# Performance work log

Measured on AMD Instinct MI355X. Metric: run time of the kernel, lower is better.

## Reference

```python
import jax, jax.numpy as jnp
import numpy as np

N, D, H = 1024, 256, 512


def _linear_init(key, fan_in, fan_out):
    kw, kb = jax.random.split(key)
    bound = 1.0 / np.sqrt(fan_in)
    w = jax.random.uniform(kw, (fan_in, fan_out), jnp.float32, -bound, bound)
    b = jax.random.uniform(kb, (fan_out,), jnp.float32, -bound, bound)
    return w, b


def setup_inputs() -> dict:
    key = jax.random.key(0)
    ks = jax.random.split(key, 8)
    domain_a = jax.random.normal(ks[0], (N, D), jnp.float32)
    domain_b = jax.random.normal(ks[1], (N, D), jnp.float32)
    mu_w0, mu_b0 = _linear_init(ks[2], D, H)
    mu_w1, mu_b1 = _linear_init(ks[3], H, H)
    mu_w2, mu_b2 = _linear_init(ks[4], H, D)
    lv_w0, lv_b0 = _linear_init(ks[5], D, H)
    lv_w1, lv_b1 = _linear_init(ks[6], H, H)
    lv_w2, lv_b2 = _linear_init(ks[7], H, D)
    return dict(domain_a=domain_a, domain_b=domain_b,
                mu_w0=mu_w0, mu_b0=mu_b0, mu_w1=mu_w1, mu_b1=mu_b1, mu_w2=mu_w2, mu_b2=mu_b2,
                lv_w0=lv_w0, lv_b0=lv_b0, lv_w1=lv_w1, lv_b1=lv_b1, lv_w2=lv_w2, lv_b2=lv_b2)


def _net(x, ws, bs, final_act):
    h = x
    for i in range(len(ws)):
        h = h @ ws[i] + bs[i]
        if i < len(ws) - 1:
            h = jax.nn.relu(h)
    return final_act(h)


def _l2norm(h):
    # L2NormEncoder == F.normalize(dim=-1), eps clamp like torch
    n = jnp.maximum(jnp.linalg.norm(h, axis=-1, keepdims=True), 1e-12)
    return h / n


def reference(domain_a, domain_b, mu_w0, mu_b0, mu_w1, mu_b1, mu_w2, mu_b2,
              lv_w0, lv_b0, lv_w1, lv_b1, lv_w2, lv_b2):
    mu_ws, mu_bs = [mu_w0, mu_w1, mu_w2], [mu_b0, mu_b1, mu_b2]
    lv_ws, lv_bs = [lv_w0, lv_w1, lv_w2], [lv_b0, lv_b1, lv_b2]

    # ---- embedding-model loss: prob-model params frozen (requires_grad=False) ----
    sg = jax.lax.stop_gradient
    mu = _net(domain_a, [sg(w) for w in mu_ws], [sg(b) for b in mu_bs], _l2norm)
    log_var = _net(domain_a, [sg(w) for w in lv_ws], [sg(b) for b in lv_bs], jnp.tanh)
    inv_var = jnp.exp(-log_var)                                  # [N, D]
    pos_probs = jnp.sum(-(domain_b - mu) ** 2 * inv_var - log_var, axis=-1)  # [N]
    # pairwise: [i, j, d] = b[j, d] - mu[i, d]; mean over j
    diff2_mean = jnp.mean((domain_b[None, :, :] - mu[:, None, :]) ** 2, axis=1)  # [N, D]
    neg_probs = jnp.sum(-diff2_mean * inv_var - log_var, axis=-1)  # [N]
    embed_model_loss = jnp.mean(pos_probs - neg_probs)

    # ---- prob-model loss: embeddings detached, params trainable ----
    a_d, b_d = sg(domain_a), sg(domain_b)
    mu2 = _net(a_d, mu_ws, mu_bs, _l2norm)
    lv2 = _net(a_d, lv_ws, lv_bs, jnp.tanh)
    prob_model_loss = jnp.mean(jnp.sum((b_d - mu2) ** 2 * jnp.exp(-lv2) + lv2, axis=-1))

    emb_coef, prob_coef = 1.0, 1.0
    loss = emb_coef * embed_model_loss + prob_coef * prob_model_loss
    return loss
```

## Files before the change

kernel.cpp:

```cpp
#include <hip/hip_runtime.h>
#include <hip/hip_fp16.h>

#define N_ROWS 1024
#define DIM 256
#define HID 512
#define CTR 16

typedef _Float16 half_t;
typedef __attribute__((ext_vector_type(4))) _Float16 half4v;
typedef __attribute__((ext_vector_type(8))) _Float16 half8v;
typedef __attribute__((ext_vector_type(16))) float f32x16;

struct Params {
    const float* a;
    const float* b;
    const float* w[6];
    const float* bias[6];
    unsigned* c1;
    unsigned* c2;
    unsigned* c3;
    float* acc;
    unsigned* done;
    float* zbase;
    float* part_s;
    float* part_s2;
    unsigned short* g_mu;
    unsigned short* g_lv;
    half_t* g_h1[2];
    half_t* g_h2[2];
    half_t* wt[6];
    float* out;
};

__global__ __launch_bounds__(256) void prep_kernel(Params p) {
    const int y = blockIdx.y, bx = blockIdx.x, tid = threadIdx.x;

    if (y == 6) {
        if (bx < 64) {
            const int d = tid, r0 = bx * 16;
            float s = 0.f, s2 = 0.f;
            #pragma unroll
            for (int r = 0; r < 16; ++r) {
                float v = p.b[(r0 + r) * DIM + d];
                s += v; s2 = fmaf(v, v, s2);
            }
            p.part_s[bx * 256 + d] = s;
            p.part_s2[bx * 256 + d] = s2;
        } else if (bx == 64) {
            #pragma unroll
            for (int k = 0; k < 12; ++k) p.zbase[tid + k * 256] = 0.f;
        }
        return;
    }
    __shared__ float T[32][33];
    const float* src = p.w[y];
    half_t* dst = p.wt[y];
    const int K = (y < 2) ? DIM : HID;
    const int N = (y < 4) ? HID : DIM;
    const int C = K >> 5;
    const int tilesN = N >> 5;
    if (bx >= C * tilesN) return;
    const int tk = bx / tilesN, tn = bx % tilesN;

    {
        const int r = tid >> 3, c4 = (tid & 7) * 4;
        float4 v = *(const float4*)&src[(tk * 32 + r) * N + tn * 32 + c4];
        T[r][c4 + 0] = v.x; T[r][c4 + 1] = v.y; T[r][c4 + 2] = v.z; T[r][c4 + 3] = v.w;
    }
    __syncthreads();
    const int which = tid >> 7;
    const int lane64 = (tid >> 1) & 63;
    const int epart = tid & 1;
    const int hi = lane64 >> 5, lr = lane64 & 31;
    const int rbase = which * 16 + hi * 8 + epart * 4;
    half4v h;
    h[0] = (half_t)T[rbase + 0][lr];
    h[1] = (half_t)T[rbase + 1][lr];
    h[2] = (half_t)T[rbase + 2][lr];
    h[3] = (half_t)T[rbase + 3][lr];
    *(half4v*)&dst[((tn * C + tk) * 2 + which) * 512 + lane64 * 8 + epart * 4] = h;
}

__device__ __forceinline__ void flag_add_wave(unsigned* c) {
    asm volatile("s_waitcnt vmcnt(0)" ::: "memory");
    if ((threadIdx.x & 63) == 0)
        __hip_atomic_fetch_add(c, 1u, __ATOMIC_RELAXED, __HIP_MEMORY_SCOPE_AGENT);
}
__device__ __forceinline__ void flag_wait(unsigned* c, unsigned tgt) {
    if (threadIdx.x == 0) {
        while (__hip_atomic_load(c, __ATOMIC_RELAXED, __HIP_MEMORY_SCOPE_AGENT) < tgt)
            __builtin_amdgcn_s_sleep(1);
    }
    __syncthreads();
    asm volatile("" ::: "memory");
}

template <int KC, int PRE>
__device__ __forceinline__ f32x16 mma_pre(const half_t* __restrict__ Ap0,
                                          const half_t* __restrict__ Wp,
                                          const half8v (*wpre)[2], const int lane) {
    const int lr = lane & 31, hi = lane >> 5;
    const int sa = (lr >> 3) & 3;
    const int aoff0 = lr * 40 + ((hi ^ sa) * 8);
    const int aoff1 = lr * 40 + (((hi + 2) ^ sa) * 8);
    f32x16 acc;
    #pragma unroll
    for (int i = 0; i < 16; ++i) acc[i] = 0.f;
    #pragma unroll
    for (int c = 0; c < KC; ++c) {
        half8v av0 = *(const half8v*)(Ap0 + c * 1280 + aoff0);
        half8v av1 = *(const half8v*)(Ap0 + c * 1280 + aoff1);
        half8v bv0 = (c < PRE) ? wpre[c][0] : *(const half8v*)(Wp + c * 1024);
        half8v bv1 = (c < PRE) ? wpre[c][1] : *(const half8v*)(Wp + c * 1024 + 512);
        acc = __builtin_amdgcn_mfma_f32_32x32x16_f16(av0, bv0, acc, 0, 0, 0);
        acc = __builtin_amdgcn_mfma_f32_32x32x16_f16(av1, bv1, acc, 0, 0, 0);
    }
    return acc;
}

__device__ __forceinline__ void stage_a(const float* __restrict__ a, half_t* XA,
                                        const int R0, const int tid) {
    const int r = tid >> 4, q = tid & 15;
    const float* src = &a[(R0 + r) * DIM + q * 16];
    float4 v0 = *(const float4*)(src);
    float4 v1 = *(const float4*)(src + 4);
    float4 v2 = *(const float4*)(src + 8);
    float4 v3 = *(const float4*)(src + 12);
    half8v h0, h1;
    h0[0] = (half_t)v0.x; h0[1] = (half_t)v0.y; h0[2] = (half_t)v0.z; h0[3] = (half_t)v0.w;
    h0[4] = (half_t)v1.x; h0[5] = (half_t)v1.y; h0[6] = (half_t)v1.z; h0[7] = (half_t)v1.w;
    h1[0] = (half_t)v2.x; h1[1] = (half_t)v2.y; h1[2] = (half_t)v2.z; h1[3] = (half_t)v2.w;
    h1[4] = (half_t)v3.x; h1[5] = (half_t)v3.y; h1[6] = (half_t)v3.z; h1[7] = (half_t)v3.w;
    const int c = q >> 1, kb0 = (q & 1) * 2, sr = (r >> 3) & 3;
    *(half8v*)&XA[c * 1280 + r * 40 + ((kb0 ^ sr) * 8)] = h0;
    *(half8v*)&XA[c * 1280 + r * 40 + (((kb0 + 1) ^ sr) * 8)] = h1;
}

__device__ __forceinline__ void stage_h(const half_t* __restrict__ src, half_t* XA,
                                        const int R0, const int tid) {
    const int r = tid >> 4, q = tid & 15;
    const half_t* sp = &src[(R0 + r) * HID + q * 32];
    half8v x0 = *(const half8v*)(sp);
    half8v x1 = *(const half8v*)(sp + 8);
    half8v x2 = *(const half8v*)(sp + 16);
    half8v x3 = *(const half8v*)(sp + 24);
    const int sr = (r >> 3) & 3;
    half_t* d = &XA[q * 1280 + r * 40];
    *(half8v*)&d[(0 ^ sr) * 8] = x0;
    *(half8v*)&d[(1 ^ sr) * 8] = x1;
    *(half8v*)&d[(2 ^ sr) * 8] = x2;
    *(half8v*)&d[(3 ^ sr) * 8] = x3;
}

#define OFF_REDH  24576
#define OFF_EB    41024
#define OFF_BSUM  43072

__device__ __forceinline__ void reduce2_wide(f32x16 acc, char* smem, int tl, int kh,
                                             int lane, int tid,
                                             const float* __restrict__ bias, int colbase,
                                             unsigned short* __restrict__ dstG,
                                             int R0, bool relu) {
    float* redf = (float*)smem;
    half_t* redh = (half_t*)(smem + OFF_REDH);
    __syncthreads();
    if (kh) {
        #pragma unroll
        for (int i = 0; i < 16; ++i) redf[tl * 1024 + i * 64 + lane] = acc[i];
    }
    __syncthreads();
    if (!kh) {
        const int lr = lane & 31, hi = lane >> 5;
        const int coll = tl * 32 + lr;
        const float bv = bias[colbase + coll];
        #pragma unroll
        for (int i = 0; i < 16; ++i) {
            float v = acc[i] + redf[tl * 1024 + i * 64 + lane] + bv;
            if (relu) v = fmaxf(v, 0.f);
            const int row = (i & 3) + 8 * (i >> 2) + 4 * hi;
            redh[row * 136 + coll] = (half_t)v;
        }
    }
    __syncthreads();
    {
        const int row = tid >> 4, c8 = (tid & 15) * 8;
        const unsigned long long* sp = (const unsigned long long*)&redh[row * 136 + c8];
        unsigned long long v0 = sp[0], v1 = sp[1];
        unsigned long long* dp = (unsigned long long*)&dstG[(R0 + row) * HID + colbase + c8];
        __hip_atomic_store(dp, v0, __ATOMIC_RELAXED, __HIP_MEMORY_SCOPE_AGENT);
        __hip_atomic_store(dp + 1, v1, __ATOMIC_RELAXED, __HIP_MEMORY_SCOPE_AGENT);
    }
}

__device__ __forceinline__ void reduce4_wide(f32x16 acc, char* smem, int tl, int kq,
                                             int lane, int tid,
                                             const float* __restrict__ bias, int colbase,
                                             unsigned short* __restrict__ dstG,
                                             int R0) {
    float* redf = (float*)smem;
    half_t* redh = (half_t*)(smem + OFF_REDH);
    __syncthreads();
    if (kq) {
        #pragma unroll
        for (int i = 0; i < 16; ++i)
            redf[(tl * 3 + kq - 1) * 1024 + i * 64 + lane] = acc[i];
    }
    __syncthreads();
    if (!kq) {
        const int lr = lane & 31, hi = lane >> 5;
        const int coll = tl * 32 + lr;
        const float bv = bias[colbase + coll];
        #pragma unroll
        for (int i = 0; i < 16; ++i) {
            float v = acc[i] + bv
                    + redf[(tl * 3 + 0) * 1024 + i * 64 + lane]
                    + redf[(tl * 3 + 1) * 1024 + i * 64 + lane]
                    + redf[(tl * 3 + 2) * 1024 + i * 64 + lane];
            const int row = (i & 3) + 8 * (i >> 2) + 4 * hi;
            redh[row * 72 + coll] = (half_t)v;
        }
    }
    __syncthreads();
    {
        const int row = tid >> 4, c4 = (tid & 15) * 4;
        unsigned long long v0 = *(const unsigned long long*)&redh[row * 72 + c4];
        unsigned long long* dp = (unsigned long long*)&dstG[(R0 + row) * DIM + colbase + c4];
        __hip_atomic_store(dp, v0, __ATOMIC_RELAXED, __HIP_MEMORY_SCOPE_AGENT);
    }
}

__global__ void __launch_bounds__(512) main_kernel(Params p) {
    __shared__ alignas(16) char smem[43136];
    half_t* XA = (half_t*)smem;
    float* ebL  = (float*)(smem + OFF_EB);
    float* eb2L = ebL + 256;
    float* bsum = (float*)(smem + OFF_BSUM);

    const int bid = blockIdx.x, tid = threadIdx.x;
    const int net = bid & 1, g = (bid >> 1) & 31, s = bid >> 6;
    const int R0 = g * 32;
    const int w = tid >> 6, lane = tid & 63;

    half8v wpre[4][2];

    stage_a(p.a, XA, R0, tid);
    __syncthreads();
    {
        const int tl = w >> 1, kh = w & 1;
        const half_t* Wp = p.wt[net] + ((s * 4 + tl) * 8 + kh * 4) * 1024 + lane * 8;
        f32x16 acc = mma_pre<4, 0>(XA + kh * 4 * 1280, Wp, nullptr, lane);
        reduce2_wide(acc, smem, tl, kh, lane, tid, p.bias[net], s * 128,
                     (unsigned short*)p.g_h1[net], R0, true);
    }
    flag_add_wave(p.c1 + (net * 32 + g) * CTR);

    const int tl2 = w >> 1, kh2 = w & 1;
    const half_t* WpL1 = p.wt[2 + net] + ((s * 4 + tl2) * 16 + kh2 * 8) * 1024 + lane * 8;
    #pragma unroll
    for (int c = 0; c < 4; ++c) {
        wpre[c][0] = *(const half8v*)(WpL1 + c * 1024);
        wpre[c][1] = *(const half8v*)(WpL1 + c * 1024 + 512);
    }
    flag_wait(p.c1 + (net * 32 + g) * CTR, 32);
    stage_h(p.g_h1[net], XA, R0, tid);
    __syncthreads();
    {
        f32x16 acc = mma_pre<8, 4>(XA + kh2 * 8 * 1280, WpL1, wpre, lane);
        reduce2_wide(acc, smem, tl2, kh2, lane, tid, p.bias[2 + net], s * 128,
                     (unsigned short*)p.g_h2[net], R0, true);
    }
    flag_add_wave(p.c2 + (net * 32 + g) * CTR);

    const int tl3 = w >> 2, kq3 = w & 3;
    const half_t* WpL2 = p.wt[4 + net] + ((s * 2 + tl3) * 16 + kq3 * 4) * 1024 + lane * 8;
    #pragma unroll
    for (int c = 0; c < 4; ++c) {
        wpre[c][0] = *(const half8v*)(WpL2 + c * 1024);
        wpre[c][1] = *(const half8v*)(WpL2 + c * 1024 + 512);
    }
    flag_wait(p.c2 + (net * 32 + g) * CTR, 32);
    stage_h(p.g_h2[net], XA, R0, tid);
    __syncthreads();
    {
        f32x16 acc = mma_pre<4, 4>(XA + kq3 * 4 * 1280, WpL2, wpre, lane);
        reduce4_wide(acc, smem, tl3, kq3, lane, tid, p.bias[4 + net], s * 64,
                     net ? p.g_lv : p.g_mu, R0);
    }
    flag_add_wave(p.c3 + g * CTR);

    if (net == 0) return;

    if (tid == 0) *bsum = 0.f;
    {
        const int which = tid >> 8, d = tid & 255;
        const float* P = which ? p.part_s2 : p.part_s;
        float ssum = 0.f;
        #pragma unroll 8
        for (int j = 0; j < 64; ++j) ssum += P[j * 256 + d];
        (which ? eb2L : ebL)[d] = ssum * (1.0f / (float)N_ROWS);
    }
    flag_wait(p.c3 + g * CTR, 64);

    const int i = R0 + s * 8 + w;
    const int d0 = lane * 4;
    const half_t* muP = (const half_t*)p.g_mu;
    const half_t* lvP = (const half_t*)p.g_lv;
    half4v mh = *(const half4v*)&muP[i * DIM + d0];
    half4v lh = *(const half4v*)&lvP[i * DIM + d0];
    float4 ebf = *(const float4*)&ebL[d0];
    float4 eb2f = *(const float4*)&eb2L[d0];
    float m4[4] = {(float)mh[0], (float)mh[1], (float)mh[2], (float)mh[3]};
    float l4[4] = {(float)lh[0], (float)lh[1], (float)lh[2], (float)lh[3]};
    float eb[4] = {ebf.x, ebf.y, ebf.z, ebf.w};
    float eb2[4] = {eb2f.x, eb2f.y, eb2f.z, eb2f.w};

    float ss = 0.f;
    #pragma unroll
    for (int t = 0; t < 4; ++t) ss = fmaf(m4[t], m4[t], ss);
    #pragma unroll
    for (int o = 32; o > 0; o >>= 1) ss += __shfl_xor(ss, o, 64);
    const float inv_norm = 1.f / fmaxf(sqrtf(ss), 1e-12f);

    float wacc = 0.f;
    #pragma unroll
    for (int t = 0; t < 4; ++t) {
        float mu = m4[t] * inv_norm;
        float lv = tanhf(l4[t]);
        float iv = expf(-lv);
        float diff2 = fmaf(mu, mu, fmaf(-2.f * mu, eb[t], eb2[t]));
        wacc += fmaf(diff2, iv, lv);
    }
    #pragma unroll
    for (int o = 32; o > 0; o >>= 1) wacc += __shfl_xor(wacc, o, 64);
    if (lane == 0) atomicAdd(bsum, wacc);
    __syncthreads();
    if (tid == 0) {
        atomicAdd(p.acc, *bsum);
        asm volatile("s_waitcnt vmcnt(0)" ::: "memory");
        unsigned prev = __hip_atomic_fetch_add(p.done, 1u, __ATOMIC_RELAXED,
                                               __HIP_MEMORY_SCOPE_AGENT);
        if (prev == 127u) {
            float v = __hip_atomic_load(p.acc, __ATOMIC_RELAXED, __HIP_MEMORY_SCOPE_AGENT);
            p.out[0] = v * (1.0f / (float)N_ROWS);
        }
    }
}

extern "C" void kernel_launch(void* const* d_in, const int* in_sizes, int n_in,
                              void* d_out, int out_size, void* d_ws, size_t ws_size,
                              hipStream_t stream) {
    Params p;
    p.a = (const float*)d_in[0];
    p.b = (const float*)d_in[1];
    p.w[0] = (const float*)d_in[2];  p.bias[0] = (const float*)d_in[3];
    p.w[2] = (const float*)d_in[4];  p.bias[2] = (const float*)d_in[5];
    p.w[4] = (const float*)d_in[6];  p.bias[4] = (const float*)d_in[7];
    p.w[1] = (const float*)d_in[8];  p.bias[1] = (const float*)d_in[9];
    p.w[3] = (const float*)d_in[10]; p.bias[3] = (const float*)d_in[11];
    p.w[5] = (const float*)d_in[12]; p.bias[5] = (const float*)d_in[13];

    float* f = (float*)d_ws;
    p.c1    = (unsigned*)f;
    p.c2    = (unsigned*)(f + 1024);
    p.c3    = (unsigned*)(f + 2048);
    p.acc   = f + 2560;
    p.done  = (unsigned*)(f + 2576);
    p.zbase = f;
    p.part_s  = f + 4096;
    p.part_s2 = f + 20480;
    p.g_mu = (unsigned short*)(f + 36864);
    p.g_lv = p.g_mu + N_ROWS * DIM;
    half_t* hb = (half_t*)(p.g_lv + N_ROWS * DIM);
    p.g_h1[0] = hb;  hb += N_ROWS * HID;
    p.g_h1[1] = hb;  hb += N_ROWS * HID;
    p.g_h2[0] = hb;  hb += N_ROWS * HID;
    p.g_h2[1] = hb;  hb += N_ROWS * HID;
    p.wt[0] = hb;  hb += HID * DIM;
    p.wt[1] = hb;  hb += HID * DIM;
    p.wt[2] = hb;  hb += HID * HID;
    p.wt[3] = hb;  hb += HID * HID;
    p.wt[4] = hb;  hb += DIM * HID;
    p.wt[5] = hb;  hb += DIM * HID;
    p.out = (float*)d_out;

    prep_kernel<<<dim3(256, 7), 256, 0, stream>>>(p);
    main_kernel<<<256, 512, 0, stream>>>(p);
}
```

Measured before the change: 30.08 us.

## Fuse weight packing and column stats into main kernel with flag-based sync

Removes the separate prep kernel and folds fp16 weight transposition/packing and the domain_b column-sum partials into the start of the persistent main kernel. Cross-block readiness is now signalled through atomic counters (cw0, cw12, cs) with spin-waits, and the counter area is zeroed by a hipMemsetAsync. The aim is to drop one kernel launch and its boundary, and to let layer-0 work begin once only the first weights are packed. The cost is extra spin-waiting and a grid-wide dependency that assumes all 256 blocks are co-resident.

```diff
diff --git a/kernel.cpp b/kernel.cpp
--- a/kernel.cpp
+++ b/kernel.cpp
@@ -19,9 +19,11 @@
     unsigned* c1;
     unsigned* c2;
     unsigned* c3;
+    unsigned* cw0;
+    unsigned* cw12;
+    unsigned* cs;
     float* acc;
     unsigned* done;
-    float* zbase;
     float* part_s;
     float* part_s2;
     unsigned short* g_mu;
@@ -32,55 +34,12 @@
     float* out;
 };
 
-__global__ __launch_bounds__(256) void prep_kernel(Params p) {
-    const int y = blockIdx.y, bx = blockIdx.x, tid = threadIdx.x;
-
-    if (y == 6) {
-        if (bx < 64) {
-            const int d = tid, r0 = bx * 16;
-            float s = 0.f, s2 = 0.f;
-            #pragma unroll
-            for (int r = 0; r < 16; ++r) {
-                float v = p.b[(r0 + r) * DIM + d];
-                s += v; s2 = fmaf(v, v, s2);
-            }
-            p.part_s[bx * 256 + d] = s;
-            p.part_s2[bx * 256 + d] = s2;
-        } else if (bx == 64) {
-            #pragma unroll
-            for (int k = 0; k < 12; ++k) p.zbase[tid + k * 256] = 0.f;
-        }
-        return;
-    }
-    __shared__ float T[32][33];
-    const float* src = p.w[y];
-    half_t* dst = p.wt[y];
-    const int K = (y < 2) ? DIM : HID;
-    const int N = (y < 4) ? HID : DIM;
-    const int C = K >> 5;
-    const int tilesN = N >> 5;
-    if (bx >= C * tilesN) return;
-    const int tk = bx / tilesN, tn = bx % tilesN;
-
-    {
-        const int r = tid >> 3, c4 = (tid & 7) * 4;
-        float4 v = *(const float4*)&src[(tk * 32 + r) * N + tn * 32 + c4];
-        T[r][c4 + 0] = v.x; T[r][c4 + 1] = v.y; T[r][c4 + 2] = v.z; T[r][c4 + 3] = v.w;
-    }
-    __syncthreads();
-    const int which = tid >> 7;
-    const int lane64 = (tid >> 1) & 63;
-    const int epart = tid & 1;
-    const int hi = lane64 >> 5, lr = lane64 & 31;
-    const int rbase = which * 16 + hi * 8 + epart * 4;
-    half4v h;
-    h[0] = (half_t)T[rbase + 0][lr];
-    h[1] = (half_t)T[rbase + 1][lr];
-    h[2] = (half_t)T[rbase + 2][lr];
-    h[3] = (half_t)T[rbase + 3][lr];
-    *(half4v*)&dst[((tn * C + tk) * 2 + which) * 512 + lane64 * 8 + epart * 4] = h;
-}
-
+__device__ __forceinline__ void flag_add(unsigned* c) {
+    asm volatile("s_waitcnt vmcnt(0)" ::: "memory");
+    __syncthreads();
+    if (threadIdx.x == 0)
+        __hip_atomic_fetch_add(c, 1u, __ATOMIC_RELAXED, __HIP_MEMORY_SCOPE_AGENT);
+}
 __device__ __forceinline__ void flag_add_wave(unsigned* c) {
     asm volatile("s_waitcnt vmcnt(0)" ::: "memory");
     if ((threadIdx.x & 63) == 0)
@@ -93,6 +52,38 @@
     }
     __syncthreads();
     asm volatile("" ::: "memory");
+}
+
+__device__ __forceinline__ void pack_round(const float* __restrict__ src,
+                                           half_t* __restrict__ dst,
+                                           int K, int N, int tk, int tn,
+                                           char* smem, bool active) {
+    float (*T)[33] = (float(*)[33])(smem + (threadIdx.x >> 8) * 4352);
+    const int t = threadIdx.x & 255;
+    const int r = t >> 3, c4 = (t & 7) * 4;
+    if (active) {
+        float4 v = *(const float4*)&src[(tk * 32 + r) * N + tn * 32 + c4];
+        T[r][c4 + 0] = v.x; T[r][c4 + 1] = v.y; T[r][c4 + 2] = v.z; T[r][c4 + 3] = v.w;
+    }
+    __syncthreads();
+    if (active) {
+        const int which = t >> 7;
+        const int lane64 = (t >> 1) & 63;
+        const int epart = t & 1;
+        const int hi = lane64 >> 5, lr = lane64 & 31;
+        const int rbase = which * 16 + hi * 8 + epart * 4;
+        half4v h;
+        h[0] = (half_t)T[rbase + 0][lr];
+        h[1] = (half_t)T[rbase + 1][lr];
+        h[2] = (half_t)T[rbase + 2][lr];
+        h[3] = (half_t)T[rbase + 3][lr];
+        const int C = K >> 5;
+        union { half4v h4; unsigned long long u; } cv; cv.h4 = h;
+        __hip_atomic_store(
+            (unsigned long long*)&dst[((tn * C + tk) * 2 + which) * 512 + lane64 * 8 + epart * 4],
+            cv.u, __ATOMIC_RELAXED, __HIP_MEMORY_SCOPE_AGENT);
+    }
+    __syncthreads();
 }
 
 template <int KC, int PRE>
@@ -241,21 +232,60 @@
     const int R0 = g * 32;
     const int w = tid >> 6, lane = tid & 63;
 
+    {
+        const int y = bid >> 7, rr = bid & 127;
+        pack_round(p.w[y], p.wt[y], DIM, HID, rr >> 4, rr & 15, smem, tid < 256);
+    }
+    flag_add(p.cw0);
+    {
+        const int gid = bid * 2 + (tid >> 8);
+        const int y = 2 + (gid >> 8), rr = gid & 255;
+        pack_round(p.w[y], p.wt[y], HID, HID, rr >> 4, rr & 15, smem, true);
+    }
+    {
+        const int y = 4 + (bid >> 7), rr = bid & 127;
+        pack_round(p.w[y], p.wt[y], HID, DIM, rr >> 3, rr & 7, smem, tid < 256);
+    }
+    flag_add(p.cw12);
+
+    if (bid < 64) {
+        if (tid < 256) {
+            const int d = tid, r0 = bid * 16;
+            float s0 = 0.f, s2 = 0.f;
+            #pragma unroll
+            for (int r = 0; r < 16; ++r) {
+                float v = p.b[(r0 + r) * DIM + d];
+                s0 += v; s2 = fmaf(v, v, s2);
+            }
+            __hip_atomic_store(&p.part_s[bid * 256 + d], s0, __ATOMIC_RELAXED,
+                               __HIP_MEMORY_SCOPE_AGENT);
+            __hip_atomic_store(&p.part_s2[bid * 256 + d], s2, __ATOMIC_RELAXED,
+                               __HIP_MEMORY_SCOPE_AGENT);
+        }
+        flag_add(p.cs);
+    }
+
     half8v wpre[4][2];
 
     stage_a(p.a, XA, R0, tid);
-    __syncthreads();
-    {
-        const int tl = w >> 1, kh = w & 1;
-        const half_t* Wp = p.wt[net] + ((s * 4 + tl) * 8 + kh * 4) * 1024 + lane * 8;
-        f32x16 acc = mma_pre<4, 0>(XA + kh * 4 * 1280, Wp, nullptr, lane);
-        reduce2_wide(acc, smem, tl, kh, lane, tid, p.bias[net], s * 128,
+    const int tl0 = w >> 1, kh0 = w & 1;
+    const half_t* WpL0 = p.wt[net] + ((s * 4 + tl0) * 8 + kh0 * 4) * 1024 + lane * 8;
+    flag_wait(p.cw0, 256);
+    #pragma unroll
+    for (int c = 0; c < 4; ++c) {
+        wpre[c][0] = *(const half8v*)(WpL0 + c * 1024);
+        wpre[c][1] = *(const half8v*)(WpL0 + c * 1024 + 512);
+    }
+    {
+        f32x16 acc = mma_pre<4, 4>(XA + kh0 * 4 * 1280, WpL0, wpre, lane);
+        reduce2_wide(acc, smem, tl0, kh0, lane, tid, p.bias[net], s * 128,
                      (unsigned short*)p.g_h1[net], R0, true);
     }
     flag_add_wave(p.c1 + (net * 32 + g) * CTR);
 
     const int tl2 = w >> 1, kh2 = w & 1;
     const half_t* WpL1 = p.wt[2 + net] + ((s * 4 + tl2) * 16 + kh2 * 8) * 1024 + lane * 8;
+    flag_wait(p.cw12, 256);
     #pragma unroll
     for (int c = 0; c < 4; ++c) {
         wpre[c][0] = *(const half8v*)(WpL1 + c * 1024);
@@ -291,6 +321,7 @@
     if (net == 0) return;
 
     if (tid == 0) *bsum = 0.f;
+    flag_wait(p.cs, 64);
     {
         const int which = tid >> 8, d = tid & 255;
         const float* P = which ? p.part_s2 : p.part_s;
@@ -360,12 +391,14 @@
     p.w[5] = (const float*)d_in[12]; p.bias[5] = (const float*)d_in[13];
 
     float* f = (float*)d_ws;
-    p.c1    = (unsigned*)f;
-    p.c2    = (unsigned*)(f + 1024);
-    p.c3    = (unsigned*)(f + 2048);
-    p.acc   = f + 2560;
-    p.done  = (unsigned*)(f + 2576);
-    p.zbase = f;
+    p.c1   = (unsigned*)f;
+    p.c2   = (unsigned*)(f + 1024);
+    p.c3   = (unsigned*)(f + 2048);
+    p.cw0  = (unsigned*)(f + 2560);
+    p.cw12 = (unsigned*)(f + 2576);
+    p.cs   = (unsigned*)(f + 2592);
+    p.acc  = f + 2608;
+    p.done = (unsigned*)(f + 2624);
     p.part_s  = f + 4096;
     p.part_s2 = f + 20480;
     p.g_mu = (unsigned short*)(f + 36864);
@@ -383,6 +416,6 @@
     p.wt[5] = hb;  hb += DIM * HID;
     p.out = (float*)d_out;
 
-    prep_kernel<<<dim3(256, 7), 256, 0, stream>>>(p);
+    hipMemsetAsync(d_ws, 0, 12288, stream);
     main_kernel<<<256, 512, 0, stream>>>(p);
 }
```

Measured after the change: 41.36 us. 37.5% more time.
